# Optimization experiments

Hardware: AMD Instinct MI355X
Metric: run time of the kernel (lower is better)

The kernel has to match this reference:

```python
import jax, jax.numpy as jnp
import numpy as np

STRIDE = 1  # module init arg


def setup_inputs() -> dict:
    key = jax.random.key(0)
    k1, k2 = jax.random.split(key)
    x = jax.random.normal(k1, (16, 32, 256, 256), dtype=jnp.float32)
    kernel = jax.random.normal(k2, (32, 5, 5), dtype=jnp.float32) * 0.1
    return {"input": x, "kernel": kernel}


def _maxmin_conv(x, kernel, stride=STRIDE):
    # Max-min semifield convolution:
    #   out[b,oc,i,j] = max_{c,dy,dx} min(x_pad[b,c,i*s+dy,j*s+dx], k[oc,dy,dx])
    # Since min(., k) is monotone in x, the max over in-channels commutes:
    #   max_{c} min(x_c, k) == min(max_c x_c, k)
    # so we reduce channels once up front (same math, far less memory).
    K = kernel.shape[-1]
    p = K - 1
    top = p // 2
    bot = p - top  # calculate_padding(): left=top=floor(p/2), right=bottom=p-top
    xmax = jnp.max(x, axis=1)  # [B, H, W]
    xp = jnp.pad(xmax, ((0, 0), (top, bot), (top, bot)), constant_values=-np.inf)
    B, Hp, Wp = xp.shape
    Ho = (Hp - K) // stride + 1
    Wo = (Wp - K) // stride + 1
    OC = kernel.shape[0]
    acc = jnp.full((B, OC, Ho, Wo), -np.inf, dtype=x.dtype)
    for dy in range(K):  # fixed small K*K loop over kernel taps
        for dx in range(K):
            patch = xp[:, dy:dy + stride * Ho:stride, dx:dx + stride * Wo:stride]  # [B,Ho,Wo]
            cand = jnp.minimum(patch[:, None, :, :], kernel[None, :, dy, dx, None, None])
            acc = jnp.maximum(acc, cand)
    return acc


def reference(input, kernel):
    return _maxmin_conv(input, kernel)
```

## Files before the change

### kernel.cpp

```cpp
#include <hip/hip_runtime.h>
#include <math.h>


#define BATCH 16
#define CH    32
#define OCH   32
#define HH    256
#define WW    256
#define HWSZ  (HH * WW)
#define TW    32
#define TH    16
#define LH    20
#define LW    42
#define NWG   (BATCH * (HH / TH) * (WW / TW))

typedef float floatx4 __attribute__((ext_vector_type(4)));

__global__ void sort_taps_kernel(const float* __restrict__ kk, float2* __restrict__ ent) {
    int t = threadIdx.x;
    if (t >= OCH * 25) return;
    int oc = t / 25, i = t % 25;
    float ki = kk[oc * 25 + i];
    int rank = 0;
#pragma unroll
    for (int j = 0; j < 25; ++j) {
        float kj = kk[oc * 25 + j];
        rank += (kj > ki) || (kj == ki && j < i);
    }
    int dy = i / 5, dx = i % 5;
    int off = 4 * (dy * LW + dx);
    ent[oc * 26 + rank] = make_float2(ki, __int_as_float(off));
    if (i == 0) ent[oc * 26 + 25] = make_float2(-INFINITY, __int_as_float(0));
}

__global__ __launch_bounds__(256, 2) void fused_maxmin_kernel(const float* __restrict__ x,
                                                              const float2* __restrict__ gent,
                                                              float* __restrict__ out) {
    __shared__ float xmt[LH][LW];
    __shared__ float2 ent[OCH * 26];
    int tid = threadIdx.x;
    int bid = blockIdx.x;
    int swz = (bid & 7) * (NWG >> 3) + (bid >> 3);
    int b   = swz >> 7;
    int t2  = swz & 127;
    int ty  = t2 >> 3;
    int tx  = t2 & 7;

    const float NI = -INFINITY;

    for (int i = tid; i < OCH * 26; i += 256) ent[i] = gent[i];

    if (tid < 200) {
        int pr = tid / 10;
        int pc = tid % 10;
        int c4 = tx * 8 - 1 + pc;
        int rw = ty * TH - 2 + pr;
        bool valid = (c4 >= 0) && (c4 < WW / 4) && (rw >= 0) && (rw < HH);
        int c4c = c4 < 0 ? 0 : (c4 > WW / 4 - 1 ? WW / 4 - 1 : c4);
        int rwc = rw < 0 ? 0 : (rw > HH - 1 ? HH - 1 : rw);
        const float4* src = (const float4*)x + (size_t)b * CH * (HWSZ / 4)
                          + (size_t)rwc * (WW / 4) + c4c;
        float4 m = src[0];
#pragma unroll
        for (int c = 1; c < CH; ++c) {
            float4 v = src[(size_t)c * (HWSZ / 4)];
            m.x = fmaxf(m.x, v.x);
            m.y = fmaxf(m.y, v.y);
            m.z = fmaxf(m.z, v.z);
            m.w = fmaxf(m.w, v.w);
        }
        if (!valid) { m.x = NI; m.y = NI; m.z = NI; m.w = NI; }
        *(float2*)&xmt[pr][4 * pc]     = make_float2(m.x, m.y);
        *(float2*)&xmt[pr][4 * pc + 2] = make_float2(m.z, m.w);
    }
    __syncthreads();

    int xg = tid & 7;
    int rg = (tid >> 3) & 7;
    int wv = __builtin_amdgcn_readfirstlane(tid >> 6);

    const char* r0p = (const char*)&xmt[2 * rg][4 * xg + 2];
    const char* r1p = (const char*)&xmt[2 * rg + 1][4 * xg + 2];

    size_t obase = (size_t)(b * OCH + wv * 8) * HWSZ
                 + (size_t)(ty * TH + 2 * rg) * WW + tx * TW + 4 * xg;

    for (int o = 0; o < 8; ++o) {
        const float2* E = &ent[(wv * 8 + o) * 26];
        float a00 = NI, a01 = NI, a02 = NI, a03 = NI;
        float a10 = NI, a11 = NI, a12 = NI, a13 = NI;

        for (int i = 0; i < 25; ++i) {
            float2 e  = E[i];
            float  kn = E[i + 1].x;
            float  kv = e.x;
            int    off = __float_as_int(e.y);
            const float* p0 = (const float*)(r0p + off);
            const float* p1 = (const float*)(r1p + off);
            a00 = fmaxf(a00, fminf(p0[0], kv));
            a01 = fmaxf(a01, fminf(p0[1], kv));
            a02 = fmaxf(a02, fminf(p0[2], kv));
            a03 = fmaxf(a03, fminf(p0[3], kv));
            a10 = fmaxf(a10, fminf(p1[0], kv));
            a11 = fmaxf(a11, fminf(p1[1], kv));
            a12 = fmaxf(a12, fminf(p1[2], kv));
            a13 = fmaxf(a13, fminf(p1[3], kv));
            float mn = fminf(fminf(fminf(a00, a01), fminf(a02, a03)),
                             fminf(fminf(a10, a11), fminf(a12, a13)));
            if (__all(mn >= kn)) break;
        }

        float* op = out + obase + (size_t)o * HWSZ;
        floatx4 o0 = { a00, a01, a02, a03 };
        floatx4 o1 = { a10, a11, a12, a13 };
        __builtin_nontemporal_store(o0, (floatx4*)op);
        __builtin_nontemporal_store(o1, (floatx4*)(op + WW));
    }
}

extern "C" void kernel_launch(void* const* d_in, const int* in_sizes, int n_in,
                              void* d_out, int out_size, void* d_ws, size_t ws_size,
                              hipStream_t stream) {
    const float* x  = (const float*)d_in[0];
    const float* kk = (const float*)d_in[1];
    float* out      = (float*)d_out;
    float2* ent     = (float2*)d_ws;

    sort_taps_kernel<<<1, OCH * 25, 0, stream>>>(kk, ent);
    fused_maxmin_kernel<<<NWG, 256, 0, stream>>>(x, ent, out);
}
```

Before: 54.55 us.

## Split channel-max reduction into separate kernel with batched loads

Moves the 32-channel max reduction out of the fused conv kernel into its own kernel that writes a reduced [B,H,W] plane to workspace, issuing 16 outstanding float4 loads per batch. This removes the redundant halo re-reads of all 32 channels per tile (each tile read a 20x40 region over 32 channels) and lets the reduction run with more memory-level parallelism. In exchange it adds a kernel launch and a 4MB intermediate write and read.

```diff
diff --git a/kernel.cpp b/kernel.cpp
--- a/kernel.cpp
+++ b/kernel.cpp
@@ -12,7 +12,7 @@
 #define TH    16
 #define LH    20
 #define LW    42
-#define NWG   (BATCH * (HH / TH) * (WW / TW))
+#define NWGB  (BATCH * (HH / TH) * (WW / TW))
 
 typedef float floatx4 __attribute__((ext_vector_type(4)));
 
@@ -33,14 +33,40 @@
     if (i == 0) ent[oc * 26 + 25] = make_float2(-INFINITY, __int_as_float(0));
 }
 
-__global__ __launch_bounds__(256, 2) void fused_maxmin_kernel(const float* __restrict__ x,
-                                                              const float2* __restrict__ gent,
-                                                              float* __restrict__ out) {
+__global__ __launch_bounds__(256) void chanmax_kernel(const float* __restrict__ x,
+                                                      float* __restrict__ xm) {
+    int i4 = blockIdx.x * blockDim.x + threadIdx.x;
+    int b  = i4 >> 14;
+    int r  = i4 & 16383;
+    const float4* base = (const float4*)x + (size_t)b * (CH * (HWSZ / 4)) + r;
+
+    float4 v[16];
+#pragma unroll
+    for (int j = 0; j < 16; ++j) v[j] = base[(size_t)j * (HWSZ / 4)];
+    float4 m = v[0];
+#pragma unroll
+    for (int j = 1; j < 16; ++j) {
+        m.x = fmaxf(m.x, v[j].x); m.y = fmaxf(m.y, v[j].y);
+        m.z = fmaxf(m.z, v[j].z); m.w = fmaxf(m.w, v[j].w);
+    }
+#pragma unroll
+    for (int j = 0; j < 16; ++j) v[j] = base[(size_t)(16 + j) * (HWSZ / 4)];
+#pragma unroll
+    for (int j = 0; j < 16; ++j) {
+        m.x = fmaxf(m.x, v[j].x); m.y = fmaxf(m.y, v[j].y);
+        m.z = fmaxf(m.z, v[j].z); m.w = fmaxf(m.w, v[j].w);
+    }
+    ((float4*)xm)[i4] = m;
+}
+
+__global__ __launch_bounds__(256, 2) void conv_kernel(const float* __restrict__ xm,
+                                                      const float2* __restrict__ gent,
+                                                      float* __restrict__ out) {
     __shared__ float xmt[LH][LW];
     __shared__ float2 ent[OCH * 26];
     int tid = threadIdx.x;
     int bid = blockIdx.x;
-    int swz = (bid & 7) * (NWG >> 3) + (bid >> 3);
+    int swz = (bid & 7) * (NWGB >> 3) + (bid >> 3);
     int b   = swz >> 7;
     int t2  = swz & 127;
     int ty  = t2 >> 3;
@@ -58,17 +84,8 @@
         bool valid = (c4 >= 0) && (c4 < WW / 4) && (rw >= 0) && (rw < HH);
         int c4c = c4 < 0 ? 0 : (c4 > WW / 4 - 1 ? WW / 4 - 1 : c4);
         int rwc = rw < 0 ? 0 : (rw > HH - 1 ? HH - 1 : rw);
-        const float4* src = (const float4*)x + (size_t)b * CH * (HWSZ / 4)
-                          + (size_t)rwc * (WW / 4) + c4c;
-        float4 m = src[0];
-#pragma unroll
-        for (int c = 1; c < CH; ++c) {
-            float4 v = src[(size_t)c * (HWSZ / 4)];
-            m.x = fmaxf(m.x, v.x);
-            m.y = fmaxf(m.y, v.y);
-            m.z = fmaxf(m.z, v.z);
-            m.w = fmaxf(m.w, v.w);
-        }
+        float4 m = *((const float4*)xm + (size_t)b * (HWSZ / 4)
+                     + (size_t)rwc * (WW / 4) + c4c);
         if (!valid) { m.x = NI; m.y = NI; m.z = NI; m.w = NI; }
         *(float2*)&xmt[pr][4 * pc]     = make_float2(m.x, m.y);
         *(float2*)&xmt[pr][4 * pc + 2] = make_float2(m.z, m.w);
@@ -125,7 +142,9 @@
     const float* kk = (const float*)d_in[1];
     float* out      = (float*)d_out;
     float2* ent     = (float2*)d_ws;
+    float*  xm      = (float*)((char*)d_ws + 8192);
 
     sort_taps_kernel<<<1, OCH * 25, 0, stream>>>(kk, ent);
-    fused_maxmin_kernel<<<NWG, 256, 0, stream>>>(x, ent, out);
+    chanmax_kernel<<<BATCH * HWSZ / 4 / 256, 256, 0, stream>>>(x, xm);
+    conv_kernel<<<NWGB, 256, 0, stream>>>(xm, ent, out);
 }
```

Result: slower. 64.02 us (+17.4%).
